# Performance work log

Hardware: AMD Instinct MI355X
Metric: run time of the kernel (lower is better)

Reference implementation:

```python
import jax, jax.numpy as jnp
import numpy as np
import math

B, L, D, H = 16, 144, 512, 8
DH = D // H          # 64, equals structure feature dim
DS, HS = 64, 8       # structure sub-attention model dim / heads
DFF = 2048

def ln(x, g, b, eps=1e-6):
    m = jnp.mean(x, -1, keepdims=True)
    v = jnp.mean((x - m) ** 2, -1, keepdims=True)
    return (x - m) * jax.lax.rsqrt(v + eps) * g + b

def setup_inputs():
    key = jax.random.key(0)
    ks = iter(jax.random.split(key, 32))
    def w(shape, s=0.02):
        return jax.random.normal(next(ks), shape, jnp.float32) * s
    return {
        "inputs": jax.random.normal(next(ks), (B, L, D), jnp.float32),
        "structure": jax.random.normal(next(ks), (L * L, 4, B, DS), jnp.float32),
        "mask": jax.random.randint(next(ks), (B, L, L), 0, 2, jnp.int32),
        "g_att": jnp.ones((D,), jnp.float32), "b_att": jnp.zeros((D,), jnp.float32),
        "Wq": w((D, D)), "bq": jnp.zeros((D,), jnp.float32),
        "Wk": w((D, D)), "bk": jnp.zeros((D,), jnp.float32),
        "Wv": w((D, D)), "bv": jnp.zeros((D,), jnp.float32),
        "Wo": w((D, D)), "bo": jnp.zeros((D,), jnp.float32),
        "sWq": w((DS, DS)), "sbq": jnp.zeros((DS,), jnp.float32),
        "sWk": w((DS, DS)), "sbk": jnp.zeros((DS,), jnp.float32),
        "sWv": w((DS, DS)), "sbv": jnp.zeros((DS,), jnp.float32),
        "sWo": w((DS, DS)), "sbo": jnp.zeros((DS,), jnp.float32),
        "Wc": w((DS, DS, 4)), "bc": jnp.zeros((DS,), jnp.float32),
        "g_s": jnp.ones((DS,), jnp.float32), "b_s": jnp.zeros((DS,), jnp.float32),
        "g_ffn": jnp.ones((D,), jnp.float32), "b_ffn": jnp.zeros((D,), jnp.float32),
        "W1": w((D, DFF)), "b1": jnp.zeros((DFF,), jnp.float32),
        "W2": w((DFF, D)), "b2": jnp.zeros((D,), jnp.float32),
    }

def _forward(inputs, structure, mask, g_att, b_att, Wq, bq, Wk, bk, Wv, bv, Wo, bo,
             sWq, sbq, sWk, sbk, sWv, sbv, sWo, sbo, Wc, bc, g_s, b_s,
             g_ffn, b_ffn, W1, b1, W2, b2):
    x_norm = ln(inputs, g_att, b_att)

    # --- structure pipeline: [L*L,4,B,DS] -> (transpose(0,1),transpose(0,2)) -> [B,L*L,4,DS] -> [N,4,DS]
    N = B * L * L
    s = jnp.transpose(structure, (2, 0, 1, 3)).reshape(N, 4, DS)
    dsh = DS // HS
    def split_s(t):
        return t.reshape(N, 4, HS, dsh).transpose(0, 2, 1, 3)
    q = split_s(s @ sWq + sbq) / math.sqrt(dsh)
    k = split_s(s @ sWk + sbk)
    v = split_s(s @ sWv + sbv)
    attn = jax.nn.softmax(jnp.einsum('nhid,nhjd->nhij', q, k), -1)
    ctx = jnp.einsum('nhij,nhjd->nhid', attn, v).transpose(0, 2, 1, 3).reshape(N, 4, DS)
    sa = ctx @ sWo + sbo                                  # [N,4,DS]
    # Conv1d(64,64,kernel=4) over the length-4 axis (valid -> length 1) + ReLU
    conv = jax.nn.relu(jnp.einsum('ntc,oct->no', sa, Wc) + bc)  # [N,DS]
    R = ln(conv.reshape(B, L, L, DS), g_s, b_s)           # per-pair relation embeddings

    # --- relation-aware self-attention (structure added to keys and values)
    def split_h(t):
        return t.reshape(B, L, H, DH).transpose(0, 2, 1, 3)
    q = split_h(x_norm @ Wq + bq) / math.sqrt(DH)
    k = split_h(x_norm @ Wk + bk)
    v = split_h(x_norm @ Wv + bv)
    scores = jnp.einsum('bhid,bhjd->bhij', q, k) + jnp.einsum('bhid,bijd->bhij', q, R)
    scores = jnp.where(mask[:, None, :, :] != 0, jnp.float32(-1e18), scores)
    attn = jax.nn.softmax(scores, -1)
    ctx = jnp.einsum('bhij,bhjd->bhid', attn, v) + jnp.einsum('bhij,bijd->bhid', attn, R)
    ctx = ctx.transpose(0, 2, 1, 3).reshape(B, L, D)
    x = ctx @ Wo + bo + inputs

    # --- FFN (pre-LN, residual outside)
    h = jax.nn.relu(ln(x, g_ffn, b_ffn) @ W1 + b1)
    return h @ W2 + b2 + x

def reference(inputs, structure, mask, g_att, b_att, Wq, bq, Wk, bk, Wv, bv, Wo, bo,
              sWq, sbq, sWk, sbk, sWv, sbv, sWo, sbo, Wc, bc, g_s, b_s,
              g_ffn, b_ffn, W1, b1, W2, b2):
    return _forward(inputs, structure, mask, g_att, b_att, Wq, bq, Wk, bk, Wv, bv, Wo, bo,
                    sWq, sbq, sWk, sbk, sWv, sbv, sWo, sbo, Wc, bc, g_s, b_s,
                    g_ffn, b_ffn, W1, b1, W2, b2)
```

## Files before the change

kernel.cpp:

```cpp
#include <hip/hip_runtime.h>
#include <math.h>


typedef __bf16 bf16_t;
typedef __bf16 bf16x8 __attribute__((ext_vector_type(8)));
typedef __bf16 bf16x4 __attribute__((ext_vector_type(4)));
typedef __bf16 bf16x2v __attribute__((ext_vector_type(2)));
typedef float f32x4 __attribute__((ext_vector_type(4)));

__global__ __launch_bounds__(256) void transpose_all(
    const float* __restrict__ Wq, const float* __restrict__ Wk,
    const float* __restrict__ Wv, const float* __restrict__ Wo,
    const float* __restrict__ W1, const float* __restrict__ W2,
    bf16_t* __restrict__ WqkvT, bf16_t* __restrict__ WoT,
    bf16_t* __restrict__ W1T, bf16_t* __restrict__ W2T) {
  int bid = blockIdx.x;
  const float* W; bf16_t* WT; int K, N; float scale = 1.f; int tile;
  if (bid < 256)       { W = Wq; WT = WqkvT;            K = 512;  N = 512;  scale = 0.125f; tile = bid; }
  else if (bid < 512)  { W = Wk; WT = WqkvT + 262144;   K = 512;  N = 512;  tile = bid - 256; }
  else if (bid < 768)  { W = Wv; WT = WqkvT + 524288;   K = 512;  N = 512;  tile = bid - 512; }
  else if (bid < 1024) { W = Wo; WT = WoT;              K = 512;  N = 512;  tile = bid - 768; }
  else if (bid < 2048) { W = W1; WT = W1T;              K = 512;  N = 2048; tile = bid - 1024; }
  else                 { W = W2; WT = W2T;              K = 2048; N = 512;  tile = bid - 2048; }
  int ntn = N >> 5;
  int nb = (tile % ntn) * 32, kb = (tile / ntn) * 32;
  __shared__ float t32[32][33];
  int tx = threadIdx.x & 31, ty = threadIdx.x >> 5;
#pragma unroll
  for (int i = ty; i < 32; i += 8) t32[i][tx] = W[(size_t)(kb + i) * N + nb + tx];
  __syncthreads();
#pragma unroll
  for (int i = ty; i < 32; i += 8)
    WT[(size_t)(nb + i) * K + kb + tx] = (__bf16)(t32[tx][i] * scale);
}

__global__ __launch_bounds__(256) void precompute_misc(
    const float* __restrict__ sWq, const float* __restrict__ sWk,
    const float* __restrict__ sWv, const float* __restrict__ sWo,
    const float* __restrict__ sbq, const float* __restrict__ sbk,
    const float* __restrict__ sbv, const float* __restrict__ sbo,
    const float* __restrict__ Wc, const float* __restrict__ bc,
    const float* __restrict__ bq, const float* __restrict__ bk,
    const float* __restrict__ bv, bf16_t* __restrict__ WT3,
    bf16_t* __restrict__ M2T, float* __restrict__ C0,
    float* __restrict__ sbqkv, float* __restrict__ bqkv) {
  int blk = blockIdx.x, tid = threadIdx.x;
  if (blk == 16) {
    const float qs = 0.35355339059327373f;
    for (int idx = tid; idx < 4096; idx += 256) {
      int j = idx >> 6, ic = idx & 63;
      int cj = (j & 7) * 8 + 2 * ((j >> 4) & 3) + ((j >> 3) & 1);
      WT3[idx] = (__bf16)(sWq[ic * 64 + cj] * qs);
      WT3[4096 + idx] = (__bf16)sWk[ic * 64 + cj];
      WT3[8192 + idx] = (__bf16)sWv[ic * 64 + cj];
    }
    if (tid < 64) {
      float s = bc[tid];
      for (int c = 0; c < 64; ++c) {
        float sb = sbo[c];
#pragma unroll
        for (int t = 0; t < 4; ++t) s += sb * Wc[tid * 256 + c * 4 + t];
      }
      C0[tid] = s;
      int cj = (tid & 7) * 8 + 2 * ((tid >> 4) & 3) + ((tid >> 3) & 1);
      sbqkv[tid] = sbq[cj] * qs;
      sbqkv[64 + tid] = sbk[cj];
      sbqkv[128 + tid] = sbv[cj];
    }
  } else if (blk == 17) {
    for (int i = tid; i < 1536; i += 256)
      bqkv[i] = (i < 512) ? bq[i] * 0.125f
                          : ((i < 1024) ? bk[i - 512] : bv[i - 1024]);
  } else {
    int t = blk >> 2;
    int e = (blk & 3) * 16 + (tid >> 4);
    int o4 = (tid & 15) * 4;
    float acc[4] = {0.f, 0.f, 0.f, 0.f};
    for (int c = 0; c < 64; ++c) {
      float a = sWo[e * 64 + c];
#pragma unroll
      for (int j = 0; j < 4; ++j) acc[j] += a * Wc[(o4 + j) * 256 + c * 4 + t];
    }
#pragma unroll
    for (int j = 0; j < 4; ++j)
      M2T[(o4 + j) * 256 + t * 64 + e] = (__bf16)acc[j];
  }
}

__global__ __launch_bounds__(256) void ln512(
    const float* __restrict__ x, const float* __restrict__ g,
    const float* __restrict__ bb, bf16_t* __restrict__ out) {
  int row = blockIdx.x, tid = threadIdx.x;
  const float* xr = x + (size_t)row * 512;
  float2 v = *(const float2*)&xr[tid * 2];
  float s1 = v.x + v.y;
  float s2 = v.x * v.x + v.y * v.y;
#pragma unroll
  for (int m = 32; m >= 1; m >>= 1) {
    s1 += __shfl_xor(s1, m);
    s2 += __shfl_xor(s2, m);
  }
  __shared__ float red[8];
  int wid = tid >> 6;
  if ((tid & 63) == 0) { red[wid * 2] = s1; red[wid * 2 + 1] = s2; }
  __syncthreads();
  s1 = red[0] + red[2] + red[4] + red[6];
  s2 = red[1] + red[3] + red[5] + red[7];
  float mean = s1 * (1.f / 512.f);
  float var = s2 * (1.f / 512.f) - mean * mean;
  float rs = 1.f / sqrtf(var + 1e-6f);
  int c = tid * 2;
  float2 gg = *(const float2*)&g[c];
  float2 bv = *(const float2*)&bb[c];
  bf16x2v o;
  o[0] = (__bf16)((v.x - mean) * rs * gg.x + bv.x);
  o[1] = (__bf16)((v.y - mean) * rs * gg.y + bv.y);
  *(bf16x2v*)&out[(size_t)row * 512 + c] = o;
}

template <int MR>
__global__ __launch_bounds__(256) void gemm_bf16(
    const bf16_t* __restrict__ A, const bf16_t* __restrict__ BT,
    const float* __restrict__ bias, const float* __restrict__ res,
    float* __restrict__ Cf, bf16_t* __restrict__ Cb, int M, int N, int K,
    int relu) {
  constexpr int RT = MR / 64;
  int tid = threadIdx.x;
  int w = tid >> 6, l = tid & 63, l15 = l & 15, l4 = l >> 4;
  int n0 = blockIdx.x * 64, m0 = blockIdx.y * MR;
  const bf16_t* Arow[RT];
#pragma unroll
  for (int rt = 0; rt < RT; ++rt)
    Arow[rt] = A + (size_t)(m0 + (w * RT + rt) * 16 + l15) * K + l4 * 8;
  const bf16_t* Bbase = BT + (size_t)(n0 + l15) * K + l4 * 8;
  f32x4 acc[RT][4];
#pragma unroll
  for (int ct = 0; ct < 4; ++ct) {
    float bv = bias[n0 + ct * 16 + l15];
#pragma unroll
    for (int rt = 0; rt < RT; ++rt) acc[rt][ct] = (f32x4){bv, bv, bv, bv};
  }
#pragma unroll 4
  for (int k0 = 0; k0 < K; k0 += 32) {
    bf16x8 a8[RT];
#pragma unroll
    for (int rt = 0; rt < RT; ++rt) a8[rt] = *(const bf16x8*)(Arow[rt] + k0);
#pragma unroll
    for (int ct = 0; ct < 4; ++ct) {
      bf16x8 b8 = *(const bf16x8*)(Bbase + (size_t)ct * 16 * K + k0);
#pragma unroll
      for (int rt = 0; rt < RT; ++rt)
        acc[rt][ct] =
            __builtin_amdgcn_mfma_f32_16x16x32_bf16(a8[rt], b8, acc[rt][ct], 0, 0, 0);
    }
  }
#pragma unroll
  for (int ct = 0; ct < 4; ++ct) {
    int col = n0 + ct * 16 + l15;
#pragma unroll
    for (int rt = 0; rt < RT; ++rt) {
#pragma unroll
      for (int i = 0; i < 4; ++i) {
        int row = m0 + (w * RT + rt) * 16 + l4 * 4 + i;
        float vv = acc[rt][ct][i];
        if (relu) vv = fmaxf(vv, 0.f);
        if (res) vv += res[(size_t)row * N + col];
        if (Cf) Cf[(size_t)row * N + col] = vv;
        if (Cb) Cb[(size_t)row * N + col] = (__bf16)vv;
      }
    }
  }
}

__global__ __launch_bounds__(256, 2) void struct_mfma(
    const float* __restrict__ S, const bf16_t* __restrict__ WT3,
    const float* __restrict__ sbqkv, const bf16_t* __restrict__ M2T,
    const float* __restrict__ C0, const float* __restrict__ gs,
    const float* __restrict__ bsv, bf16_t* __restrict__ Rout) {
  __shared__ __align__(16) char smem[67584];
  int tid = threadIdx.x;
  int w = tid >> 6, l = tid & 63, l15 = l & 15, l4 = l >> 4;
  int p0 = blockIdx.x * 4;

  bf16x8 wq[4][2], wk[4][2], wv[4][2];
  float biq[4], bik[4], biv[4];
#pragma unroll
  for (int ct = 0; ct < 4; ++ct) {
    int j = ct * 16 + l15;
#pragma unroll
    for (int kb = 0; kb < 2; ++kb) {
      int off = j * 64 + kb * 32 + l4 * 8;
      wq[ct][kb] = *(const bf16x8*)(WT3 + off);
      wk[ct][kb] = *(const bf16x8*)(WT3 + 4096 + off);
      wv[ct][kb] = *(const bf16x8*)(WT3 + 8192 + off);
    }
    biq[ct] = sbqkv[j];
    bik[ct] = sbqkv[64 + j];
    biv[ct] = sbqkv[128 + j];
  }

  {
    int row = tid >> 4;
    int cb0 = (tid & 15) * 16;
    const float* src = S + (size_t)(p0 * 4 + row) * 1024;
    int key = (row & 7) << 4;
#pragma unroll
    for (int i = 0; i < 8; ++i) {
      int colb = cb0 + i * 256;
      int c0 = colb >> 1;
      float4 u0 = *(const float4*)(src + c0);
      float4 u1 = *(const float4*)(src + c0 + 4);
      bf16x8 a;
      a[0] = (__bf16)u0.x; a[1] = (__bf16)u0.y;
      a[2] = (__bf16)u0.z; a[3] = (__bf16)u0.w;
      a[4] = (__bf16)u1.x; a[5] = (__bf16)u1.y;
      a[6] = (__bf16)u1.z; a[7] = (__bf16)u1.w;
      *(bf16x8*)(smem + row * 2048 + (colb ^ key)) = a;
    }
  }
  __syncthreads();

  int pl = l >> 4, h = l & 7, hi = (l >> 3) & 1;
#pragma unroll 1
  for (int r = 0; r < 4; ++r) {
    int b = r * 4 + w;
    int akey = (l15 & 7) << 4;
    int colb0 = b * 128 + l4 * 16;
    bf16x8 af0 = *(const bf16x8*)(smem + l15 * 2048 + (colb0 ^ akey));
    bf16x8 af1 = *(const bf16x8*)(smem + l15 * 2048 + ((colb0 + 64) ^ akey));
    f32x4 aq[4], ak[4], av[4];
#pragma unroll
    for (int ct = 0; ct < 4; ++ct) {
      aq[ct] = (f32x4){biq[ct], biq[ct], biq[ct], biq[ct]};
      ak[ct] = (f32x4){bik[ct], bik[ct], bik[ct], bik[ct]};
      av[ct] = (f32x4){biv[ct], biv[ct], biv[ct], biv[ct]};
    }
#pragma unroll
    for (int ct = 0; ct < 4; ++ct) {
      aq[ct] = __builtin_amdgcn_mfma_f32_16x16x32_bf16(af0, wq[ct][0], aq[ct], 0, 0, 0);
      aq[ct] = __builtin_amdgcn_mfma_f32_16x16x32_bf16(af1, wq[ct][1], aq[ct], 0, 0, 0);
      ak[ct] = __builtin_amdgcn_mfma_f32_16x16x32_bf16(af0, wk[ct][0], ak[ct], 0, 0, 0);
      ak[ct] = __builtin_amdgcn_mfma_f32_16x16x32_bf16(af1, wk[ct][1], ak[ct], 0, 0, 0);
      av[ct] = __builtin_amdgcn_mfma_f32_16x16x32_bf16(af0, wv[ct][0], av[ct], 0, 0, 0);
      av[ct] = __builtin_amdgcn_mfma_f32_16x16x32_bf16(af1, wv[ct][1], av[ct], 0, 0, 0);
    }
    float Sm[4][4];
#pragma unroll
    for (int i2 = 0; i2 < 4; ++i2)
#pragma unroll
      for (int j2 = 0; j2 < 4; ++j2)
        Sm[i2][j2] = aq[0][i2] * ak[0][j2] + aq[1][i2] * ak[1][j2] +
                     aq[2][i2] * ak[2][j2] + aq[3][i2] * ak[3][j2];
#pragma unroll
    for (int i2 = 0; i2 < 4; ++i2)
#pragma unroll
      for (int j2 = 0; j2 < 4; ++j2)
        Sm[i2][j2] += __shfl_xor(Sm[i2][j2], 8);
    float P[4][4], inv[4];
#pragma unroll
    for (int i2 = 0; i2 < 4; ++i2) {
      float rs = 0.f;
#pragma unroll
      for (int j2 = 0; j2 < 4; ++j2) {
        P[i2][j2] = __expf(Sm[i2][j2]);
        rs += P[i2][j2];
      }
      inv[i2] = __builtin_amdgcn_rcpf(rs);
    }
    int unit = r * 16 + w * 4 + pl;
    char* cb = smem + 32768 + unit * 544;
    int ckey = (unit & 7) << 4;
#pragma unroll
    for (int ct = 0; ct < 4; ++ct) {
      int c = h * 8 + 2 * ct + hi;
#pragma unroll
      for (int i2 = 0; i2 < 4; ++i2) {
        float cx = (P[i2][0] * av[ct][0] + P[i2][1] * av[ct][1] +
                    P[i2][2] * av[ct][2] + P[i2][3] * av[ct][3]) * inv[i2];
        *(bf16_t*)(cb + ((i2 * 128 + c * 2) ^ ckey)) = (__bf16)cx;
      }
    }
  }
  __syncthreads();

  float* cvp = (float*)smem;
  {
    bf16x8 ax[8];
    int rkey = (l15 & 7) << 4;
    char* cbase = smem + 32768 + (w * 16 + l15) * 544;
#pragma unroll
    for (int kb = 0; kb < 8; ++kb) {
      int byt = (kb >> 1) * 128 + (kb & 1) * 64 + l4 * 16;
      ax[kb] = *(const bf16x8*)(cbase + (byt ^ rkey));
    }
#pragma unroll 1
    for (int ct = 0; ct < 4; ++ct) {
      int o = ct * 16 + l15;
      float c0v = C0[o];
      f32x4 acc = (f32x4){c0v, c0v, c0v, c0v};
#pragma unroll
      for (int kb = 0; kb < 8; ++kb) {
        bf16x8 mf = *(const bf16x8*)(M2T + o * 256 + kb * 32 + l4 * 8);
        acc = __builtin_amdgcn_mfma_f32_16x16x32_bf16(ax[kb], mf, acc, 0, 0, 0);
      }
#pragma unroll
      for (int i2 = 0; i2 < 4; ++i2)
        cvp[(w * 16 + l4 * 4 + i2) * 68 + o] = fmaxf(acc[i2], 0.f);
    }
  }
  __syncthreads();

  {
    int unit = tid >> 2, ch0 = (tid & 3) * 16;
    const float* cr = cvp + unit * 68 + ch0;
    float4 v0 = *(const float4*)(cr);
    float4 v1 = *(const float4*)(cr + 4);
    float4 v2 = *(const float4*)(cr + 8);
    float4 v3 = *(const float4*)(cr + 12);
    float s1 = v0.x + v0.y + v0.z + v0.w + v1.x + v1.y + v1.z + v1.w +
               v2.x + v2.y + v2.z + v2.w + v3.x + v3.y + v3.z + v3.w;
    float s2 = v0.x * v0.x + v0.y * v0.y + v0.z * v0.z + v0.w * v0.w +
               v1.x * v1.x + v1.y * v1.y + v1.z * v1.z + v1.w * v1.w +
               v2.x * v2.x + v2.y * v2.y + v2.z * v2.z + v2.w * v2.w +
               v3.x * v3.x + v3.y * v3.y + v3.z * v3.z + v3.w * v3.w;
    s1 += __shfl_xor(s1, 1); s1 += __shfl_xor(s1, 2);
    s2 += __shfl_xor(s2, 1); s2 += __shfl_xor(s2, 2);
    float mean = s1 * (1.f / 64.f);
    float var = s2 * (1.f / 64.f) - mean * mean;
    float rstd = 1.f / sqrtf(var + 1e-6f);
    float4 g0 = *(const float4*)&gs[ch0];
    float4 g1 = *(const float4*)&gs[ch0 + 4];
    float4 g2 = *(const float4*)&gs[ch0 + 8];
    float4 g3 = *(const float4*)&gs[ch0 + 12];
    float4 b0 = *(const float4*)&bsv[ch0];
    float4 b1 = *(const float4*)&bsv[ch0 + 4];
    float4 b2 = *(const float4*)&bsv[ch0 + 8];
    float4 b3 = *(const float4*)&bsv[ch0 + 12];
    bf16x8 o0, o1;
    o0[0] = (__bf16)((v0.x - mean) * rstd * g0.x + b0.x);
    o0[1] = (__bf16)((v0.y - mean) * rstd * g0.y + b0.y);
    o0[2] = (__bf16)((v0.z - mean) * rstd * g0.z + b0.z);
    o0[3] = (__bf16)((v0.w - mean) * rstd * g0.w + b0.w);
    o0[4] = (__bf16)((v1.x - mean) * rstd * g1.x + b1.x);
    o0[5] = (__bf16)((v1.y - mean) * rstd * g1.y + b1.y);
    o0[6] = (__bf16)((v1.z - mean) * rstd * g1.z + b1.z);
    o0[7] = (__bf16)((v1.w - mean) * rstd * g1.w + b1.w);
    o1[0] = (__bf16)((v2.x - mean) * rstd * g2.x + b2.x);
    o1[1] = (__bf16)((v2.y - mean) * rstd * g2.y + b2.y);
    o1[2] = (__bf16)((v2.z - mean) * rstd * g2.z + b2.z);
    o1[3] = (__bf16)((v2.w - mean) * rstd * g2.w + b2.w);
    o1[4] = (__bf16)((v3.x - mean) * rstd * g3.x + b3.x);
    o1[5] = (__bf16)((v3.y - mean) * rstd * g3.y + b3.y);
    o1[6] = (__bf16)((v3.z - mean) * rstd * g3.z + b3.z);
    o1[7] = (__bf16)((v3.w - mean) * rstd * g3.w + b3.w);
    int rr = unit >> 4, w2 = (unit >> 2) & 3, pu = unit & 3;
    int b = rr * 4 + w2;
    size_t base = ((size_t)b * 20736 + p0 + pu) * 64 + ch0;
    *(bf16x8*)&Rout[base] = o0;
    *(bf16x8*)&Rout[base + 8] = o1;
  }
}

__global__ __launch_bounds__(256) void attn_score(
    const bf16_t* __restrict__ qkv, const bf16_t* __restrict__ R,
    const int* __restrict__ msk, bf16_t* __restrict__ Pg,
    float* __restrict__ ctmp) {
  const int L = 144;
  __shared__ __align__(16) char smem[48704];
  bf16_t* qZ = (bf16_t*)smem;
  bf16_t* RT = (bf16_t*)(smem + 16640);
  bf16_t* PL = (bf16_t*)(smem + 38144);
  float* scl = (float*)(smem + 43520);
  int* mskL = (int*)(smem + 48128);

  int blk = blockIdx.x;
  int b = blk / L, i = blk - b * L;
  int tid = threadIdx.x;
  int bL = b * L;

  bf16x8 z8;
#pragma unroll
  for (int e = 0; e < 8; ++e) z8[e] = (__bf16)0.f;

  for (int idx = tid; idx < 1040; idx += 256) {
    int r = idx / 65, c8 = (idx - r * 65) * 8;
    *(bf16x8*)&qZ[r * 520 + c8] = z8;
  }
  for (int idx = tid; idx < 336; idx += 256) {
    int r = idx / 21, c8 = (idx - r * 21) * 8;
    *(bf16x8*)&PL[r * 168 + c8] = z8;
  }
  if (tid < 192) {
    int r = tid / 3, c8 = 144 + (tid - (tid / 3) * 3) * 8;
    *(bf16x8*)&RT[r * 168 + c8] = z8;
  }
  if (tid < 144) mskL[tid] = msk[(size_t)(bL + i) * 144 + tid];
  __syncthreads();

  if (tid < 64) {
    int h = tid >> 3, d8 = (tid & 7) * 8;
    bf16x8 q8 = *(const bf16x8*)&qkv[(size_t)(bL + i) * 1536 + h * 64 + d8];
    *(bf16x8*)&qZ[h * 520 + h * 64 + d8] = q8;
  }
  for (int idx = tid; idx < 1152; idx += 256) {
    int j = idx >> 3, d8 = (idx & 7) * 8;
    bf16x8 r8 = *(const bf16x8*)&R[((size_t)(bL + i) * 144 + j) * 64 + d8];
#pragma unroll
    for (int e = 0; e < 8; ++e) RT[(d8 + e) * 168 + j] = r8[e];
  }
  __syncthreads();

  int w = tid >> 6, l = tid & 63, l15 = l & 15, l4 = l >> 4;

  {
#pragma unroll 1
    for (int jt = w; jt < 9; jt += 4) {
      const bf16_t* kg =
          qkv + (size_t)(bL + jt * 16 + l15) * 1536 + 512 + l4 * 8;
      f32x4 acc = (f32x4){0.f, 0.f, 0.f, 0.f};
#pragma unroll
      for (int ks = 0; ks < 16; ++ks) {
        bf16x8 a8 = *(const bf16x8*)&qZ[l15 * 520 + ks * 32 + l4 * 8];
        bf16x8 b8 = *(const bf16x8*)(kg + ks * 32);
        acc = __builtin_amdgcn_mfma_f32_16x16x32_bf16(a8, b8, acc, 0, 0, 0);
      }
      const bf16_t* rg =
          R + ((size_t)(bL + i) * 144 + jt * 16 + l15) * 64 + l4 * 8;
      bf16x8 a0 = *(const bf16x8*)&qZ[l15 * 520 + l15 * 64 + l4 * 8];
      bf16x8 a1 = *(const bf16x8*)&qZ[l15 * 520 + l15 * 64 + 32 + l4 * 8];
      acc = __builtin_amdgcn_mfma_f32_16x16x32_bf16(a0, *(const bf16x8*)rg,
                                                    acc, 0, 0, 0);
      acc = __builtin_amdgcn_mfma_f32_16x16x32_bf16(
          a1, *(const bf16x8*)(rg + 32), acc, 0, 0, 0);
      if (l4 < 2) {
        int j = jt * 16 + l15;
        bool mm = mskL[j] != 0;
#pragma unroll
        for (int i2 = 0; i2 < 4; ++i2)
          scl[(l4 * 4 + i2) * 144 + j] = mm ? -1e18f : acc[i2];
      }
    }
  }
  __syncthreads();

  {
    int h = tid >> 5, lw = tid & 31;
    float m = -3.4e38f;
    for (int j = lw; j < 144; j += 32) m = fmaxf(m, scl[h * 144 + j]);
#pragma unroll
    for (int mm = 16; mm >= 1; mm >>= 1) m = fmaxf(m, __shfl_xor(m, mm));
    float sum = 0.f;
    for (int j = lw; j < 144; j += 32) {
      float p = __expf(scl[h * 144 + j] - m);
      scl[h * 144 + j] = p;
      sum += p;
    }
#pragma unroll
    for (int mm = 16; mm >= 1; mm >>= 1) sum += __shfl_xor(sum, mm);
    float inv = 1.f / sum;
    bf16_t* pgrow = Pg + ((size_t)(b * 8 + h) * 144 + i) * 160;
    for (int j = lw; j < 144; j += 32) {
      __bf16 pv = (__bf16)(scl[h * 144 + j] * inv);
      PL[h * 168 + j] = pv;
      pgrow[j] = pv;
    }
    if (lw < 16) pgrow[144 + lw] = (__bf16)0.f;
  }
  __syncthreads();

  {
    f32x4 acc = (f32x4){0.f, 0.f, 0.f, 0.f};
#pragma unroll
    for (int ks = 0; ks < 5; ++ks) {
      bf16x8 a8 = *(const bf16x8*)&PL[l15 * 168 + ks * 32 + l4 * 8];
      bf16x8 b8 = *(const bf16x8*)&RT[(w * 16 + l15) * 168 + ks * 32 + l4 * 8];
      acc = __builtin_amdgcn_mfma_f32_16x16x32_bf16(a8, b8, acc, 0, 0, 0);
    }
    if (l4 < 2) {
      float* crow = ctmp + (size_t)(bL + i) * 512;
#pragma unroll
      for (int i2 = 0; i2 < 4; ++i2)
        crow[(l4 * 4 + i2) * 64 + w * 16 + l15] = acc[i2];
    }
  }
}

__global__ __launch_bounds__(256) void attn_pv(
    const bf16_t* __restrict__ qkv, const bf16_t* __restrict__ Pg,
    const float* __restrict__ ctmp, bf16_t* __restrict__ ctx_out) {
  const int L = 144;
  __shared__ __align__(16) bf16_t VT[64 * 168];
  int bx = blockIdx.x;
  int bh = bx >> 2, quarter = bx & 3;
  int b = bh >> 3, h = bh & 7;
  int tid = threadIdx.x;
  int bL = b * L;

  bf16x8 z8;
#pragma unroll
  for (int e = 0; e < 8; ++e) z8[e] = (__bf16)0.f;
  for (int idx = tid; idx < 1152; idx += 256) {
    int j = idx >> 3, d8 = (idx & 7) * 8;
    bf16x8 v8 =
        *(const bf16x8*)&qkv[(size_t)(bL + j) * 1536 + 1024 + h * 64 + d8];
#pragma unroll
    for (int e = 0; e < 8; ++e) VT[(d8 + e) * 168 + j] = v8[e];
  }
  if (tid < 192) {
    int r = tid / 3, c8 = 144 + (tid - (tid / 3) * 3) * 8;
    *(bf16x8*)&VT[r * 168 + c8] = z8;
  }
  __syncthreads();

  int w = tid >> 6, l = tid & 63, l15 = l & 15, l4 = l >> 4;
  const bf16_t* pbase = Pg + (size_t)(b * 8 + h) * 144 * 160;
  const int itS[4] = {0, 3, 5, 7};
  const int itE[4] = {3, 5, 7, 9};
#pragma unroll 1
  for (int it = itS[quarter] + w; it < itE[quarter]; it += 4) {
    const bf16_t* arow = pbase + (size_t)(it * 16 + l15) * 160 + l4 * 8;
    f32x4 acc[4];
#pragma unroll
    for (int ct = 0; ct < 4; ++ct) acc[ct] = (f32x4){0.f, 0.f, 0.f, 0.f};
#pragma unroll
    for (int ks = 0; ks < 5; ++ks) {
      bf16x8 a8 = *(const bf16x8*)(arow + ks * 32);
#pragma unroll
      for (int ct = 0; ct < 4; ++ct) {
        bf16x8 b8 =
            *(const bf16x8*)&VT[(ct * 16 + l15) * 168 + ks * 32 + l4 * 8];
        acc[ct] = __builtin_amdgcn_mfma_f32_16x16x32_bf16(a8, b8, acc[ct], 0, 0, 0);
      }
    }
#pragma unroll
    for (int ct = 0; ct < 4; ++ct) {
#pragma unroll
      for (int i2 = 0; i2 < 4; ++i2) {
        int row = it * 16 + l4 * 4 + i2;
        size_t off = (size_t)(bL + row) * 512 + h * 64 + ct * 16 + l15;
        ctx_out[off] = (__bf16)(acc[ct][i2] + ctmp[off]);
      }
    }
  }
}

extern "C" void kernel_launch(void* const* d_in, const int* in_sizes, int n_in,
                              void* d_out, int out_size, void* d_ws,
                              size_t ws_size, hipStream_t stream) {
  (void)in_sizes; (void)n_in; (void)out_size; (void)ws_size;
  const float* inputs = (const float*)d_in[0];
  const float* structure = (const float*)d_in[1];
  const int* mask = (const int*)d_in[2];
  const float* g_att = (const float*)d_in[3];
  const float* b_att = (const float*)d_in[4];
  const float* Wq = (const float*)d_in[5];
  const float* bq = (const float*)d_in[6];
  const float* Wk = (const float*)d_in[7];
  const float* bk = (const float*)d_in[8];
  const float* Wv = (const float*)d_in[9];
  const float* bv = (const float*)d_in[10];
  const float* Wo = (const float*)d_in[11];
  const float* bo = (const float*)d_in[12];
  const float* sWq = (const float*)d_in[13];
  const float* sbq = (const float*)d_in[14];
  const float* sWk = (const float*)d_in[15];
  const float* sbk = (const float*)d_in[16];
  const float* sWv = (const float*)d_in[17];
  const float* sbv = (const float*)d_in[18];
  const float* sWo = (const float*)d_in[19];
  const float* sbo = (const float*)d_in[20];
  const float* Wc = (const float*)d_in[21];
  const float* bc = (const float*)d_in[22];
  const float* g_s = (const float*)d_in[23];
  const float* b_s = (const float*)d_in[24];
  const float* g_ffn = (const float*)d_in[25];
  const float* b_ffn = (const float*)d_in[26];
  const float* W1 = (const float*)d_in[27];
  const float* b1 = (const float*)d_in[28];
  const float* W2 = (const float*)d_in[29];
  const float* b2 = (const float*)d_in[30];

  char* base = (char*)d_ws;
  bf16_t* Rw = (bf16_t*)base;
  bf16_t* qkvb = (bf16_t*)(base + 42467328);
  float* xw = (float*)(base + 49545216);
  bf16_t* xnb = (bf16_t*)(base + 54263808);
  bf16_t* ctxb = (bf16_t*)(base + 56623104);
  bf16_t* hb = (bf16_t*)(base + 58982400);
  bf16_t* WqkvT = (bf16_t*)(base + 68419584);
  bf16_t* WoT = (bf16_t*)(base + 69992448);
  bf16_t* W1T = (bf16_t*)(base + 70516736);
  bf16_t* W2T = (bf16_t*)(base + 72613888);
  bf16_t* WT3 = (bf16_t*)(base + 74711040);
  bf16_t* M2T = (bf16_t*)(base + 74735616);
  float* C0w = (float*)(base + 74768384);
  float* sbqkv = (float*)(base + 74768640);
  float* bqkv = (float*)(base + 74769408);
  bf16_t* Pg = hb;
  float* ctmp = xw;
  float* out = (float*)d_out;

  transpose_all<<<3072, 256, 0, stream>>>(Wq, Wk, Wv, Wo, W1, W2, WqkvT, WoT,
                                          W1T, W2T);
  precompute_misc<<<18, 256, 0, stream>>>(sWq, sWk, sWv, sWo, sbq, sbk, sbv,
                                          sbo, Wc, bc, bq, bk, bv, WT3, M2T,
                                          C0w, sbqkv, bqkv);
  ln512<<<2304, 256, 0, stream>>>(inputs, g_att, b_att, xnb);
  gemm_bf16<128><<<dim3(24, 18), 256, 0, stream>>>(
      xnb, WqkvT, bqkv, nullptr, nullptr, qkvb, 2304, 1536, 512, 0);
  struct_mfma<<<5184, 256, 0, stream>>>(structure, WT3, sbqkv, M2T, C0w, g_s,
                                        b_s, Rw);
  attn_score<<<2304, 256, 0, stream>>>(qkvb, Rw, mask, Pg, ctmp);
  attn_pv<<<512, 256, 0, stream>>>(qkvb, Pg, ctmp, ctxb);
  gemm_bf16<64><<<dim3(8, 36), 256, 0, stream>>>(
      ctxb, WoT, bo, inputs, xw, nullptr, 2304, 512, 512, 0);
  ln512<<<2304, 256, 0, stream>>>(xw, g_ffn, b_ffn, xnb);
  gemm_bf16<128><<<dim3(32, 18), 256, 0, stream>>>(
      xnb, W1T, b1, nullptr, nullptr, hb, 2304, 2048, 512, 1);
  gemm_bf16<64><<<dim3(8, 36), 256, 0, stream>>>(
      hb, W2T, b2, xw, out, nullptr, 2304, 512, 2048, 0);
}
```

Measured before the change: 483.3 us.

## Process two structure tiles per block with register prefetch and MFMA priority hints

Each struct_mfma block now handles 8 positions instead of 4. Half of the next tile's structure input is prefetched into registers while the first tile is computed, then loaded into shared memory for the second pass. Block count is halved, which amortizes the per-block weight register loads. s_setprio hints are also wrapped around the MFMA loops in several attention kernels. The trade-off is higher register pressure from the prefetch buffer and possibly lower occupancy.

```diff
diff --git a/kernel.cpp b/kernel.cpp
--- a/kernel.cpp
+++ b/kernel.cpp
@@ -180,7 +180,7 @@
   __shared__ __align__(16) char smem[67584];
   int tid = threadIdx.x;
   int w = tid >> 6, l = tid & 63, l15 = l & 15, l4 = l >> 4;
-  int p0 = blockIdx.x * 4;
+  int p0 = blockIdx.x * 8;
 
   bf16x8 wq[4][2], wk[4][2], wv[4][2];
   float biq[4], bik[4], biv[4];
@@ -199,14 +199,15 @@
     biv[ct] = sbqkv[128 + j];
   }
 
+  int srow = tid >> 4;
+  int scb0 = (tid & 15) * 16;
+  int skey = (srow & 7) << 4;
+
   {
-    int row = tid >> 4;
-    int cb0 = (tid & 15) * 16;
-    const float* src = S + (size_t)(p0 * 4 + row) * 1024;
-    int key = (row & 7) << 4;
+    const float* src = S + (size_t)(p0 * 4 + srow) * 1024;
 #pragma unroll
     for (int i = 0; i < 8; ++i) {
-      int colb = cb0 + i * 256;
+      int colb = scb0 + i * 256;
       int c0 = colb >> 1;
       float4 u0 = *(const float4*)(src + c0);
       float4 u1 = *(const float4*)(src + c0 + 4);
@@ -215,150 +216,206 @@
       a[2] = (__bf16)u0.z; a[3] = (__bf16)u0.w;
       a[4] = (__bf16)u1.x; a[5] = (__bf16)u1.y;
       a[6] = (__bf16)u1.z; a[7] = (__bf16)u1.w;
-      *(bf16x8*)(smem + row * 2048 + (colb ^ key)) = a;
-    }
-  }
-  __syncthreads();
+      *(bf16x8*)(smem + srow * 2048 + (colb ^ skey)) = a;
+    }
+  }
+  __syncthreads();
+
+  float4 pf[8];
+  {
+    const float* src = S + (size_t)((p0 + 4) * 4 + srow) * 1024;
+#pragma unroll
+    for (int i = 0; i < 4; ++i) {
+      int c0 = (scb0 + i * 256) >> 1;
+      pf[2 * i] = *(const float4*)(src + c0);
+      pf[2 * i + 1] = *(const float4*)(src + c0 + 4);
+    }
+  }
 
   int pl = l >> 4, h = l & 7, hi = (l >> 3) & 1;
+  float* cvp = (float*)smem;
+
+  auto compute_tile = [&](int pt) {
 #pragma unroll 1
-  for (int r = 0; r < 4; ++r) {
-    int b = r * 4 + w;
-    int akey = (l15 & 7) << 4;
-    int colb0 = b * 128 + l4 * 16;
-    bf16x8 af0 = *(const bf16x8*)(smem + l15 * 2048 + (colb0 ^ akey));
-    bf16x8 af1 = *(const bf16x8*)(smem + l15 * 2048 + ((colb0 + 64) ^ akey));
-    f32x4 aq[4], ak[4], av[4];
-#pragma unroll
-    for (int ct = 0; ct < 4; ++ct) {
-      aq[ct] = (f32x4){biq[ct], biq[ct], biq[ct], biq[ct]};
-      ak[ct] = (f32x4){bik[ct], bik[ct], bik[ct], bik[ct]};
-      av[ct] = (f32x4){biv[ct], biv[ct], biv[ct], biv[ct]};
-    }
-#pragma unroll
-    for (int ct = 0; ct < 4; ++ct) {
-      aq[ct] = __builtin_amdgcn_mfma_f32_16x16x32_bf16(af0, wq[ct][0], aq[ct], 0, 0, 0);
-      aq[ct] = __builtin_amdgcn_mfma_f32_16x16x32_bf16(af1, wq[ct][1], aq[ct], 0, 0, 0);
-      ak[ct] = __builtin_amdgcn_mfma_f32_16x16x32_bf16(af0, wk[ct][0], ak[ct], 0, 0, 0);
-      ak[ct] = __builtin_amdgcn_mfma_f32_16x16x32_bf16(af1, wk[ct][1], ak[ct], 0, 0, 0);
-      av[ct] = __builtin_amdgcn_mfma_f32_16x16x32_bf16(af0, wv[ct][0], av[ct], 0, 0, 0);
-      av[ct] = __builtin_amdgcn_mfma_f32_16x16x32_bf16(af1, wv[ct][1], av[ct], 0, 0, 0);
-    }
-    float Sm[4][4];
-#pragma unroll
-    for (int i2 = 0; i2 < 4; ++i2)
-#pragma unroll
-      for (int j2 = 0; j2 < 4; ++j2)
-        Sm[i2][j2] = aq[0][i2] * ak[0][j2] + aq[1][i2] * ak[1][j2] +
-                     aq[2][i2] * ak[2][j2] + aq[3][i2] * ak[3][j2];
-#pragma unroll
-    for (int i2 = 0; i2 < 4; ++i2)
-#pragma unroll
-      for (int j2 = 0; j2 < 4; ++j2)
-        Sm[i2][j2] += __shfl_xor(Sm[i2][j2], 8);
-    float P[4][4], inv[4];
-#pragma unroll
-    for (int i2 = 0; i2 < 4; ++i2) {
-      float rs = 0.f;
-#pragma unroll
-      for (int j2 = 0; j2 < 4; ++j2) {
-        P[i2][j2] = __expf(Sm[i2][j2]);
-        rs += P[i2][j2];
-      }
-      inv[i2] = __builtin_amdgcn_rcpf(rs);
-    }
-    int unit = r * 16 + w * 4 + pl;
-    char* cb = smem + 32768 + unit * 544;
-    int ckey = (unit & 7) << 4;
-#pragma unroll
-    for (int ct = 0; ct < 4; ++ct) {
-      int c = h * 8 + 2 * ct + hi;
+    for (int r = 0; r < 4; ++r) {
+      int b = r * 4 + w;
+      int akey = (l15 & 7) << 4;
+      int colb0 = b * 128 + l4 * 16;
+      bf16x8 af0 = *(const bf16x8*)(smem + l15 * 2048 + (colb0 ^ akey));
+      bf16x8 af1 = *(const bf16x8*)(smem + l15 * 2048 + ((colb0 + 64) ^ akey));
+      f32x4 aq[4], ak[4], av[4];
+#pragma unroll
+      for (int ct = 0; ct < 4; ++ct) {
+        aq[ct] = (f32x4){biq[ct], biq[ct], biq[ct], biq[ct]};
+        ak[ct] = (f32x4){bik[ct], bik[ct], bik[ct], bik[ct]};
+        av[ct] = (f32x4){biv[ct], biv[ct], biv[ct], biv[ct]};
+      }
+      __builtin_amdgcn_s_setprio(1);
+#pragma unroll
+      for (int ct = 0; ct < 4; ++ct) {
+        aq[ct] = __builtin_amdgcn_mfma_f32_16x16x32_bf16(af0, wq[ct][0], aq[ct], 0, 0, 0);
+        aq[ct] = __builtin_amdgcn_mfma_f32_16x16x32_bf16(af1, wq[ct][1], aq[ct], 0, 0, 0);
+        ak[ct] = __builtin_amdgcn_mfma_f32_16x16x32_bf16(af0, wk[ct][0], ak[ct], 0, 0, 0);
+        ak[ct] = __builtin_amdgcn_mfma_f32_16x16x32_bf16(af1, wk[ct][1], ak[ct], 0, 0, 0);
+        av[ct] = __builtin_amdgcn_mfma_f32_16x16x32_bf16(af0, wv[ct][0], av[ct], 0, 0, 0);
+        av[ct] = __builtin_amdgcn_mfma_f32_16x16x32_bf16(af1, wv[ct][1], av[ct], 0, 0, 0);
+      }
+      __builtin_amdgcn_s_setprio(0);
+      float Sm[4][4];
+#pragma unroll
+      for (int i2 = 0; i2 < 4; ++i2)
+#pragma unroll
+        for (int j2 = 0; j2 < 4; ++j2)
+          Sm[i2][j2] = aq[0][i2] * ak[0][j2] + aq[1][i2] * ak[1][j2] +
+                       aq[2][i2] * ak[2][j2] + aq[3][i2] * ak[3][j2];
+#pragma unroll
+      for (int i2 = 0; i2 < 4; ++i2)
+#pragma unroll
+        for (int j2 = 0; j2 < 4; ++j2)
+          Sm[i2][j2] += __shfl_xor(Sm[i2][j2], 8);
+      float P[4][4], inv[4];
 #pragma unroll
       for (int i2 = 0; i2 < 4; ++i2) {
-        float cx = (P[i2][0] * av[ct][0] + P[i2][1] * av[ct][1] +
-                    P[i2][2] * av[ct][2] + P[i2][3] * av[ct][3]) * inv[i2];
-        *(bf16_t*)(cb + ((i2 * 128 + c * 2) ^ ckey)) = (__bf16)cx;
-      }
-    }
-  }
-  __syncthreads();
-
-  float* cvp = (float*)smem;
+        float rs = 0.f;
+#pragma unroll
+        for (int j2 = 0; j2 < 4; ++j2) {
+          P[i2][j2] = __expf(Sm[i2][j2]);
+          rs += P[i2][j2];
+        }
+        inv[i2] = __builtin_amdgcn_rcpf(rs);
+      }
+      int unit = r * 16 + w * 4 + pl;
+      char* cb = smem + 32768 + unit * 544;
+      int ckey = (unit & 7) << 4;
+#pragma unroll
+      for (int ct = 0; ct < 4; ++ct) {
+        int c = h * 8 + 2 * ct + hi;
+#pragma unroll
+        for (int i2 = 0; i2 < 4; ++i2) {
+          float cx = (P[i2][0] * av[ct][0] + P[i2][1] * av[ct][1] +
+                      P[i2][2] * av[ct][2] + P[i2][3] * av[ct][3]) * inv[i2];
+          *(bf16_t*)(cb + ((i2 * 128 + c * 2) ^ ckey)) = (__bf16)cx;
+        }
+      }
+    }
+    __syncthreads();
+
+    {
+      bf16x8 ax[8];
+      int rkey = (l15 & 7) << 4;
+      char* cbase = smem + 32768 + (w * 16 + l15) * 544;
+#pragma unroll
+      for (int kb = 0; kb < 8; ++kb) {
+        int byt = (kb >> 1) * 128 + (kb & 1) * 64 + l4 * 16;
+        ax[kb] = *(const bf16x8*)(cbase + (byt ^ rkey));
+      }
+#pragma unroll 1
+      for (int ct = 0; ct < 4; ++ct) {
+        int o = ct * 16 + l15;
+        float c0v = C0[o];
+        f32x4 acc = (f32x4){c0v, c0v, c0v, c0v};
+        __builtin_amdgcn_s_setprio(1);
+#pragma unroll
+        for (int kb = 0; kb < 8; ++kb) {
+          bf16x8 mf = *(const bf16x8*)(M2T + o * 256 + kb * 32 + l4 * 8);
+          acc = __builtin_amdgcn_mfma_f32_16x16x32_bf16(ax[kb], mf, acc, 0, 0, 0);
+        }
+        __builtin_amdgcn_s_setprio(0);
+#pragma unroll
+        for (int i2 = 0; i2 < 4; ++i2)
+          cvp[(w * 16 + l4 * 4 + i2) * 68 + o] = fmaxf(acc[i2], 0.f);
+      }
+    }
+    __syncthreads();
+
+    {
+      int unit = tid >> 2, ch0 = (tid & 3) * 16;
+      const float* cr = cvp + unit * 68 + ch0;
+      float4 v0 = *(const float4*)(cr);
+      float4 v1 = *(const float4*)(cr + 4);
+      float4 v2 = *(const float4*)(cr + 8);
+      float4 v3 = *(const float4*)(cr + 12);
+      float s1 = v0.x + v0.y + v0.z + v0.w + v1.x + v1.y + v1.z + v1.w +
+                 v2.x + v2.y + v2.z + v2.w + v3.x + v3.y + v3.z + v3.w;
+      float s2 = v0.x * v0.x + v0.y * v0.y + v0.z * v0.z + v0.w * v0.w +
+                 v1.x * v1.x + v1.y * v1.y + v1.z * v1.z + v1.w * v1.w +
+                 v2.x * v2.x + v2.y * v2.y + v2.z * v2.z + v2.w * v2.w +
+                 v3.x * v3.x + v3.y * v3.y + v3.z * v3.z + v3.w * v3.w;
+      s1 += __shfl_xor(s1, 1); s1 += __shfl_xor(s1, 2);
+      s2 += __shfl_xor(s2, 1); s2 += __shfl_xor(s2, 2);
+      float mean = s1 * (1.f / 64.f);
+      float var = s2 * (1.f / 64.f) - mean * mean;
+      float rstd = 1.f / sqrtf(var + 1e-6f);
+      float4 g0 = *(const float4*)&gs[ch0];
+      float4 g1 = *(const float4*)&gs[ch0 + 4];
+      float4 g2 = *(const float4*)&gs[ch0 + 8];
+      float4 g3 = *(const float4*)&gs[ch0 + 12];
+      float4 b0 = *(const float4*)&bsv[ch0];
+      float4 b1 = *(const float4*)&bsv[ch0 + 4];
+      float4 b2 = *(const float4*)&bsv[ch0 + 8];
+      float4 b3 = *(const float4*)&bsv[ch0 + 12];
+      bf16x8 o0, o1;
+      o0[0] = (__bf16)((v0.x - mean) * rstd * g0.x + b0.x);
+      o0[1] = (__bf16)((v0.y - mean) * rstd * g0.y + b0.y);
+      o0[2] = (__bf16)((v0.z - mean) * rstd * g0.z + b0.z);
+      o0[3] = (__bf16)((v0.w - mean) * rstd * g0.w + b0.w);
+      o0[4] = (__bf16)((v1.x - mean) * rstd * g1.x + b1.x);
+      o0[5] = (__bf16)((v1.y - mean) * rstd * g1.y + b1.y);
+      o0[6] = (__bf16)((v1.z - mean) * rstd * g1.z + b1.z);
+      o0[7] = (__bf16)((v1.w - mean) * rstd * g1.w + b1.w);
+      o1[0] = (__bf16)((v2.x - mean) * rstd * g2.x + b2.x);
+      o1[1] = (__bf16)((v2.y - mean) * rstd * g2.y + b2.y);
+      o1[2] = (__bf16)((v2.z - mean) * rstd * g2.z + b2.z);
+      o1[3] = (__bf16)((v2.w - mean) * rstd * g2.w + b2.w);
+      o1[4] = (__bf16)((v3.x - mean) * rstd * g3.x + b3.x);
+      o1[5] = (__bf16)((v3.y - mean) * rstd * g3.y + b3.y);
+      o1[6] = (__bf16)((v3.z - mean) * rstd * g3.z + b3.z);
+      o1[7] = (__bf16)((v3.w - mean) * rstd * g3.w + b3.w);
+      int rr = unit >> 4, w2 = (unit >> 2) & 3, pu = unit & 3;
+      int b = rr * 4 + w2;
+      size_t base = ((size_t)b * 20736 + pt + pu) * 64 + ch0;
+      *(bf16x8*)&Rout[base] = o0;
+      *(bf16x8*)&Rout[base + 8] = o1;
+    }
+  };
+
+  compute_tile(p0);
+  __syncthreads();
+
   {
-    bf16x8 ax[8];
-    int rkey = (l15 & 7) << 4;
-    char* cbase = smem + 32768 + (w * 16 + l15) * 544;
-#pragma unroll
-    for (int kb = 0; kb < 8; ++kb) {
-      int byt = (kb >> 1) * 128 + (kb & 1) * 64 + l4 * 16;
-      ax[kb] = *(const bf16x8*)(cbase + (byt ^ rkey));
-    }
-#pragma unroll 1
-    for (int ct = 0; ct < 4; ++ct) {
-      int o = ct * 16 + l15;
-      float c0v = C0[o];
-      f32x4 acc = (f32x4){c0v, c0v, c0v, c0v};
-#pragma unroll
-      for (int kb = 0; kb < 8; ++kb) {
-        bf16x8 mf = *(const bf16x8*)(M2T + o * 256 + kb * 32 + l4 * 8);
-        acc = __builtin_amdgcn_mfma_f32_16x16x32_bf16(ax[kb], mf, acc, 0, 0, 0);
-      }
-#pragma unroll
-      for (int i2 = 0; i2 < 4; ++i2)
-        cvp[(w * 16 + l4 * 4 + i2) * 68 + o] = fmaxf(acc[i2], 0.f);
-    }
-  }
-  __syncthreads();
-
-  {
-    int unit = tid >> 2, ch0 = (tid & 3) * 16;
-    const float* cr = cvp + unit * 68 + ch0;
-    float4 v0 = *(const float4*)(cr);
-    float4 v1 = *(const float4*)(cr + 4);
-    float4 v2 = *(const float4*)(cr + 8);
-    float4 v3 = *(const float4*)(cr + 12);
-    float s1 = v0.x + v0.y + v0.z + v0.w + v1.x + v1.y + v1.z + v1.w +
-               v2.x + v2.y + v2.z + v2.w + v3.x + v3.y + v3.z + v3.w;
-    float s2 = v0.x * v0.x + v0.y * v0.y + v0.z * v0.z + v0.w * v0.w +
-               v1.x * v1.x + v1.y * v1.y + v1.z * v1.z + v1.w * v1.w +
-               v2.x * v2.x + v2.y * v2.y + v2.z * v2.z + v2.w * v2.w +
-               v3.x * v3.x + v3.y * v3.y + v3.z * v3.z + v3.w * v3.w;
-    s1 += __shfl_xor(s1, 1); s1 += __shfl_xor(s1, 2);
-    s2 += __shfl_xor(s2, 1); s2 += __shfl_xor(s2, 2);
-    float mean = s1 * (1.f / 64.f);
-    float var = s2 * (1.f / 64.f) - mean * mean;
-    float rstd = 1.f / sqrtf(var + 1e-6f);
-    float4 g0 = *(const float4*)&gs[ch0];
-    float4 g1 = *(const float4*)&gs[ch0 + 4];
-    float4 g2 = *(const float4*)&gs[ch0 + 8];
-    float4 g3 = *(const float4*)&gs[ch0 + 12];
-    float4 b0 = *(const float4*)&bsv[ch0];
-    float4 b1 = *(const float4*)&bsv[ch0 + 4];
-    float4 b2 = *(const float4*)&bsv[ch0 + 8];
-    float4 b3 = *(const float4*)&bsv[ch0 + 12];
-    bf16x8 o0, o1;
-    o0[0] = (__bf16)((v0.x - mean) * rstd * g0.x + b0.x);
-    o0[1] = (__bf16)((v0.y - mean) * rstd * g0.y + b0.y);
-    o0[2] = (__bf16)((v0.z - mean) * rstd * g0.z + b0.z);
-    o0[3] = (__bf16)((v0.w - mean) * rstd * g0.w + b0.w);
-    o0[4] = (__bf16)((v1.x - mean) * rstd * g1.x + b1.x);
-    o0[5] = (__bf16)((v1.y - mean) * rstd * g1.y + b1.y);
-    o0[6] = (__bf16)((v1.z - mean) * rstd * g1.z + b1.z);
-    o0[7] = (__bf16)((v1.w - mean) * rstd * g1.w + b1.w);
-    o1[0] = (__bf16)((v2.x - mean) * rstd * g2.x + b2.x);
-    o1[1] = (__bf16)((v2.y - mean) * rstd * g2.y + b2.y);
-    o1[2] = (__bf16)((v2.z - mean) * rstd * g2.z + b2.z);
-    o1[3] = (__bf16)((v2.w - mean) * rstd * g2.w + b2.w);
-    o1[4] = (__bf16)((v3.x - mean) * rstd * g3.x + b3.x);
-    o1[5] = (__bf16)((v3.y - mean) * rstd * g3.y + b3.y);
-    o1[6] = (__bf16)((v3.z - mean) * rstd * g3.z + b3.z);
-    o1[7] = (__bf16)((v3.w - mean) * rstd * g3.w + b3.w);
-    int rr = unit >> 4, w2 = (unit >> 2) & 3, pu = unit & 3;
-    int b = rr * 4 + w2;
-    size_t base = ((size_t)b * 20736 + p0 + pu) * 64 + ch0;
-    *(bf16x8*)&Rout[base] = o0;
-    *(bf16x8*)&Rout[base + 8] = o1;
-  }
+    const float* src = S + (size_t)((p0 + 4) * 4 + srow) * 1024;
+    float4 f0[4][2];
+#pragma unroll
+    for (int i = 4; i < 8; ++i) {
+      int c0 = (scb0 + i * 256) >> 1;
+      f0[i - 4][0] = *(const float4*)(src + c0);
+      f0[i - 4][1] = *(const float4*)(src + c0 + 4);
+    }
+#pragma unroll
+    for (int i = 0; i < 4; ++i) {
+      int colb = scb0 + i * 256;
+      float4 u0 = pf[2 * i], u1 = pf[2 * i + 1];
+      bf16x8 a;
+      a[0] = (__bf16)u0.x; a[1] = (__bf16)u0.y;
+      a[2] = (__bf16)u0.z; a[3] = (__bf16)u0.w;
+      a[4] = (__bf16)u1.x; a[5] = (__bf16)u1.y;
+      a[6] = (__bf16)u1.z; a[7] = (__bf16)u1.w;
+      *(bf16x8*)(smem + srow * 2048 + (colb ^ skey)) = a;
+    }
+#pragma unroll
+    for (int i = 4; i < 8; ++i) {
+      int colb = scb0 + i * 256;
+      float4 u0 = f0[i - 4][0], u1 = f0[i - 4][1];
+      bf16x8 a;
+      a[0] = (__bf16)u0.x; a[1] = (__bf16)u0.y;
+      a[2] = (__bf16)u0.z; a[3] = (__bf16)u0.w;
+      a[4] = (__bf16)u1.x; a[5] = (__bf16)u1.y;
+      a[6] = (__bf16)u1.z; a[7] = (__bf16)u1.w;
+      *(bf16x8*)(smem + srow * 2048 + (colb ^ skey)) = a;
+    }
+  }
+  __syncthreads();
+  compute_tile(p0 + 4);
 }
 
 __global__ __launch_bounds__(256) void attn_score(
@@ -418,6 +475,7 @@
       const bf16_t* kg =
           qkv + (size_t)(bL + jt * 16 + l15) * 1536 + 512 + l4 * 8;
       f32x4 acc = (f32x4){0.f, 0.f, 0.f, 0.f};
+      __builtin_amdgcn_s_setprio(1);
 #pragma unroll
       for (int ks = 0; ks < 16; ++ks) {
         bf16x8 a8 = *(const bf16x8*)&qZ[l15 * 520 + ks * 32 + l4 * 8];
@@ -432,6 +490,7 @@
                                                     acc, 0, 0, 0);
       acc = __builtin_amdgcn_mfma_f32_16x16x32_bf16(
           a1, *(const bf16x8*)(rg + 32), acc, 0, 0, 0);
+      __builtin_amdgcn_s_setprio(0);
       if (l4 < 2) {
         int j = jt * 16 + l15;
         bool mm = mskL[j] != 0;
@@ -470,12 +529,14 @@
 
   {
     f32x4 acc = (f32x4){0.f, 0.f, 0.f, 0.f};
+    __builtin_amdgcn_s_setprio(1);
 #pragma unroll
     for (int ks = 0; ks < 5; ++ks) {
       bf16x8 a8 = *(const bf16x8*)&PL[l15 * 168 + ks * 32 + l4 * 8];
       bf16x8 b8 = *(const bf16x8*)&RT[(w * 16 + l15) * 168 + ks * 32 + l4 * 8];
       acc = __builtin_amdgcn_mfma_f32_16x16x32_bf16(a8, b8, acc, 0, 0, 0);
     }
+    __builtin_amdgcn_s_setprio(0);
     if (l4 < 2) {
       float* crow = ctmp + (size_t)(bL + i) * 512;
 #pragma unroll
@@ -522,6 +583,7 @@
     f32x4 acc[4];
 #pragma unroll
     for (int ct = 0; ct < 4; ++ct) acc[ct] = (f32x4){0.f, 0.f, 0.f, 0.f};
+    __builtin_amdgcn_s_setprio(1);
 #pragma unroll
     for (int ks = 0; ks < 5; ++ks) {
       bf16x8 a8 = *(const bf16x8*)(arow + ks * 32);
@@ -532,6 +594,7 @@
         acc[ct] = __builtin_amdgcn_mfma_f32_16x16x32_bf16(a8, b8, acc[ct], 0, 0, 0);
       }
     }
+    __builtin_amdgcn_s_setprio(0);
 #pragma unroll
     for (int ct = 0; ct < 4; ++ct) {
 #pragma unroll
@@ -608,7 +671,7 @@
   ln512<<<2304, 256, 0, stream>>>(inputs, g_att, b_att, xnb);
   gemm_bf16<128><<<dim3(24, 18), 256, 0, stream>>>(
       xnb, WqkvT, bqkv, nullptr, nullptr, qkvb, 2304, 1536, 512, 0);
-  struct_mfma<<<5184, 256, 0, stream>>>(structure, WT3, sbqkv, M2T, C0w, g_s,
+  struct_mfma<<<2592, 256, 0, stream>>>(structure, WT3, sbqkv, M2T, C0w, g_s,
                                         b_s, Rw);
   attn_score<<<2304, 256, 0, stream>>>(qkvb, Rw, mask, Pg, ctmp);
   attn_pv<<<512, 256, 0, stream>>>(qkvb, Pg, ctmp, ctxb);
```

New measurement: 550.2 us. 13.8% more time.
